# Optimization experiments

Measured on AMD Instinct MI355X. Metric: run time of the kernel, lower is better.

## Reference

```python
import math
import jax, jax.numpy as jnp
import numpy as np

B, T, C, H = 4, 2048, 1024, 16
HD = C // H  # 64


def setup_inputs() -> dict:
    key = jax.random.key(0)
    k1, k2, k3 = jax.random.split(key, 3)
    x = jax.random.normal(k1, (B, T, C), dtype=jnp.float32)
    w_attn = jax.random.normal(k2, (3 * C, C), dtype=jnp.float32) * 0.02
    w_proj = jax.random.normal(k3, (C, C), dtype=jnp.float32) * 0.02
    return {"x": x, "w_attn": w_attn, "w_proj": w_proj}


def _rms_norm(x):
    # F.rms_norm with no weight; eps defaults to dtype eps
    eps = jnp.finfo(x.dtype).eps
    return x * jax.lax.rsqrt(jnp.mean(x * x, axis=-1, keepdims=True) + eps)


def _rotary_cos_sin(seq_len, dim):
    inv_freq = 1.0 / (10000.0 ** (jnp.arange(0, dim, 2, dtype=jnp.float32) / dim))
    t = jnp.arange(seq_len, dtype=jnp.float32)
    freqs = jnp.outer(t, inv_freq)  # (T, dim//2)
    # original caches cos/sin in bfloat16
    return jnp.cos(freqs).astype(jnp.bfloat16), jnp.sin(freqs).astype(jnp.bfloat16)


def _apply_rotary(x, cos, sin):
    # x: (B, T, H, hd); cos/sin: (T, hd//2), broadcast over batch and heads
    half = x.shape[-1] // 2
    x1, x2 = x[..., :half], x[..., half:]
    c = cos[None, :, None, :].astype(x.dtype)
    s = sin[None, :, None, :].astype(x.dtype)
    y1 = x1 * c + x2 * s
    y2 = -x1 * s + x2 * c
    return jnp.concatenate([y1, y2], axis=-1)


def _forward(x, w_attn, w_proj):
    Bx, Tx, Cx = x.shape
    qkv = x @ w_attn.T  # (B, T, 3C)
    q, k, v = jnp.split(qkv, 3, axis=-1)
    q = q.reshape(Bx, Tx, H, HD)
    k = k.reshape(Bx, Tx, H, HD)
    v = v.reshape(Bx, Tx, H, HD)
    # qk RMSNorm then RoPE (nanogpt-style)
    q = _rms_norm(q)
    k = _rms_norm(k)
    cos, sin = _rotary_cos_sin(Tx, HD)
    q = _apply_rotary(q, cos, sin)
    k = _apply_rotary(k, cos, sin)
    # causal euclidean attention (custom_attention, mode='euc', dropout_p=0)
    scale = 1.0 / math.sqrt(HD)
    scores = jnp.einsum('bqhd,bkhd->bhqk', q, k) * scale  # (B, H, T, T)
    causal = jnp.tril(jnp.ones((Tx, Tx), dtype=bool))
    scores = jnp.where(causal[None, None, :, :], scores, -jnp.inf)
    attn = jax.nn.softmax(scores, axis=-1)
    y = jnp.einsum('bhqk,bkhd->bqhd', attn, v).reshape(Bx, Tx, Cx)
    return y @ w_proj.T


def reference(x, w_attn, w_proj):
    return _forward(x, w_attn, w_proj)
```

## Files before the change

kernel.cpp:

```cpp
#include <hip/hip_runtime.h>

typedef unsigned short u16;
typedef unsigned int u32;
typedef __attribute__((ext_vector_type(4))) int v4i;
typedef __attribute__((ext_vector_type(4))) float f32x4;
typedef __attribute__((ext_vector_type(16))) float f32x16;
typedef __attribute__((ext_vector_type(4))) u16 v4u;
typedef __attribute__((ext_vector_type(2))) u32 u32x2;
typedef __attribute__((ext_vector_type(8))) __bf16 bf16x8;

#define B_ 4
#define T_ 2048
#define C_ 1024
#define H_ 16
#define HD_ 64
#define C3_ 3072

__device__ __forceinline__ u16 f2b(float f) {
    unsigned u = __builtin_bit_cast(unsigned, f);
    u += 0x7FFFu + ((u >> 16) & 1u);
    return (u16)(u >> 16);
}
__device__ __forceinline__ float b2f(u16 h) {
    unsigned u = ((unsigned)h) << 16;
    return __builtin_bit_cast(float, u);
}
__device__ __forceinline__ u32 pk2(float lo, float hi) {
    __bf16 a = (__bf16)lo, b = (__bf16)hi;
    return (u32)__builtin_bit_cast(u16, a) | ((u32)__builtin_bit_cast(u16, b) << 16);
}
__device__ __forceinline__ void glds16(const u16* g, u16* l) {
    __builtin_amdgcn_global_load_lds((const __attribute__((address_space(1))) void*)g,
                                     (__attribute__((address_space(3))) void*)l, 16, 0, 0);
}

__global__ __launch_bounds__(256) void cast_f32_bf16(const float* __restrict__ in,
                                                     u16* __restrict__ out, int n4) {
    int i = blockIdx.x * 256 + threadIdx.x;
    if (i >= n4) return;
    f32x4 v = *(const f32x4*)(in + (size_t)i * 4);
    v4u o;
    o[0] = f2b(v[0]); o[1] = f2b(v[1]); o[2] = f2b(v[2]); o[3] = f2b(v[3]);
    *(v4u*)(out + (size_t)i * 4) = o;
}

__global__ __launch_bounds__(256) void rope_tab(u16* __restrict__ rope) {
    int id = blockIdx.x * 256 + threadIdx.x;
    int t = id >> 5, j = id & 31;
    float invf = exp2f(-(float)j * (13.287712379549449f / 32.0f));
    float fr = (float)t * invf;
    float s, c;
    sincosf(fr, &s, &c);
    rope[id * 2]     = f2b(c);
    rope[id * 2 + 1] = f2b(s);
}

__device__ __forceinline__ void store_out(u16* p, float v)   { *p = f2b(v); }
__device__ __forceinline__ void store_out(float* p, float v) { *p = v; }

template <typename OutT>
__global__ __launch_bounds__(256) void gemm_bt5(const u16* __restrict__ A, const u16* __restrict__ Bm,
                                                OutT* __restrict__ Cout, int Mdim, int Ndim, int Kdim) {
    __shared__ u16 As[8192];
    __shared__ u16 Bs[8192];
    const int tid = threadIdx.x;
    const int F = blockIdx.y * gridDim.x + blockIdx.x;
    const int cpx = (gridDim.x * gridDim.y) >> 3;
    const int wg = (F & 7) * cpx + (F >> 3);
    const int row0 = (wg / gridDim.x) * 128;
    const int col0 = (wg % gridDim.x) * 128;
    const int w = tid >> 6, lane = tid & 63;
    const int wm = w >> 1, wn = w & 1;
    const int lr = lane & 15, lk = lane >> 4;

    const f32x4 zf = {0.f, 0.f, 0.f, 0.f};
    f32x4 acc[4][4];
#pragma unroll
    for (int m = 0; m < 4; m++)
#pragma unroll
        for (int n = 0; n < 4; n++) acc[m][n] = zf;

    const u16* Ab = A + (size_t)row0 * Kdim;
    const u16* Bb = Bm + (size_t)col0 * Kdim;
    const int srw = lane >> 3;
    const int gch = (lane & 7) ^ (srw & 7);
    const size_t grow[4] = {
        (size_t)(w * 32 + 0 * 8 + srw) * Kdim + gch * 8,
        (size_t)(w * 32 + 1 * 8 + srw) * Kdim + gch * 8,
        (size_t)(w * 32 + 2 * 8 + srw) * Kdim + gch * 8,
        (size_t)(w * 32 + 3 * 8 + srw) * Kdim + gch * 8 };
    const int rx = lr & 7;

    for (int k0 = 0; k0 < Kdim; k0 += 64) {
#pragma unroll
        for (int j = 0; j < 4; j++) glds16(Ab + grow[j] + k0, As + (w * 32 + j * 8) * 64);
#pragma unroll
        for (int j = 0; j < 4; j++) glds16(Bb + grow[j] + k0, Bs + (w * 32 + j * 8) * 64);
        __syncthreads();
#pragma unroll
        for (int kk = 0; kk < 2; kk++) {
            const int chx = ((kk * 4 + lk) ^ rx) * 8;
            bf16x8 af[4], bfr[4];
#pragma unroll
            for (int m = 0; m < 4; m++) af[m]  = *(const bf16x8*)&As[(wm * 64 + m * 16 + lr) * 64 + chx];
#pragma unroll
            for (int n = 0; n < 4; n++) bfr[n] = *(const bf16x8*)&Bs[(wn * 64 + n * 16 + lr) * 64 + chx];
#pragma unroll
            for (int m = 0; m < 4; m++)
#pragma unroll
                for (int n = 0; n < 4; n++)
                    acc[m][n] = __builtin_amdgcn_mfma_f32_16x16x32_bf16(af[m], bfr[n], acc[m][n], 0, 0, 0);
        }
        __syncthreads();
    }
#pragma unroll
    for (int m = 0; m < 4; m++)
#pragma unroll
        for (int n = 0; n < 4; n++) {
            const int rr = row0 + wm * 64 + m * 16 + lk * 4;
            const int cc = col0 + wn * 64 + n * 16 + lr;
#pragma unroll
            for (int j = 0; j < 4; j++)
                store_out(Cout + (size_t)(rr + j) * Ndim + cc, acc[m][n][j]);
        }
}

__global__ __launch_bounds__(256) void gemm_bt6(const u16* __restrict__ A, const u16* __restrict__ Bm,
                                                float* __restrict__ Cout, int Mdim, int Ndim, int Kdim) {
    __shared__ u16 As[8192];
    __shared__ u16 Bs[4096];
    const int tid = threadIdx.x;
    const int F = blockIdx.y * gridDim.x + blockIdx.x;
    const int cpx = (gridDim.x * gridDim.y) >> 3;
    const int wg = (F & 7) * cpx + (F >> 3);
    const int row0 = (wg / gridDim.x) * 128;
    const int col0 = (wg % gridDim.x) * 64;
    const int w = tid >> 6, lane = tid & 63;
    const int wm = w >> 1, wn = w & 1;
    const int lr = lane & 15, lk = lane >> 4;

    const f32x4 zf = {0.f, 0.f, 0.f, 0.f};
    f32x4 acc[4][2];
#pragma unroll
    for (int m = 0; m < 4; m++)
#pragma unroll
        for (int n = 0; n < 2; n++) acc[m][n] = zf;

    const u16* Ab = A + (size_t)row0 * Kdim;
    const u16* Bb = Bm + (size_t)col0 * Kdim;
    const int srw = lane >> 3;
    const int gch = (lane & 7) ^ (srw & 7);
    const size_t growA[4] = {
        (size_t)(w * 32 + 0 * 8 + srw) * Kdim + gch * 8,
        (size_t)(w * 32 + 1 * 8 + srw) * Kdim + gch * 8,
        (size_t)(w * 32 + 2 * 8 + srw) * Kdim + gch * 8,
        (size_t)(w * 32 + 3 * 8 + srw) * Kdim + gch * 8 };
    const size_t growB[2] = {
        (size_t)(w * 16 + 0 * 8 + srw) * Kdim + gch * 8,
        (size_t)(w * 16 + 1 * 8 + srw) * Kdim + gch * 8 };
    const int rx = lr & 7;

    for (int k0 = 0; k0 < Kdim; k0 += 64) {
#pragma unroll
        for (int j = 0; j < 4; j++) glds16(Ab + growA[j] + k0, As + (w * 32 + j * 8) * 64);
#pragma unroll
        for (int j = 0; j < 2; j++) glds16(Bb + growB[j] + k0, Bs + (w * 16 + j * 8) * 64);
        __syncthreads();
#pragma unroll
        for (int kk = 0; kk < 2; kk++) {
            const int chx = ((kk * 4 + lk) ^ rx) * 8;
            bf16x8 af[4], bfr[2];
#pragma unroll
            for (int m = 0; m < 4; m++) af[m]  = *(const bf16x8*)&As[(wm * 64 + m * 16 + lr) * 64 + chx];
#pragma unroll
            for (int n = 0; n < 2; n++) bfr[n] = *(const bf16x8*)&Bs[(wn * 32 + n * 16 + lr) * 64 + chx];
#pragma unroll
            for (int m = 0; m < 4; m++)
#pragma unroll
                for (int n = 0; n < 2; n++)
                    acc[m][n] = __builtin_amdgcn_mfma_f32_16x16x32_bf16(af[m], bfr[n], acc[m][n], 0, 0, 0);
        }
        __syncthreads();
    }
#pragma unroll
    for (int m = 0; m < 4; m++)
#pragma unroll
        for (int n = 0; n < 2; n++) {
            const int rr = row0 + wm * 64 + m * 16 + lk * 4;
            const int cc = col0 + wn * 32 + n * 16 + lr;
#pragma unroll
            for (int j = 0; j < 4; j++)
                Cout[(size_t)(rr + j) * Ndim + cc] = acc[m][n][j];
        }
}

__global__ __launch_bounds__(256) void norm_rope3(const u16* __restrict__ qkv, u16* __restrict__ Qn,
                                                  u16* __restrict__ Kn, u16* __restrict__ Vt,
                                                  const u16* __restrict__ rope) {
    __shared__ u16 sl[32][72];
    const int tid = threadIdx.x, bid = blockIdx.x;
    const int tt = bid & 63, bh = bid >> 6;
    const int b = bh >> 4, h = bh & 15;
    const int rl = tid >> 3, g = tid & 7;
    const int t = tt * 32 + rl;
    const size_t rowbase = ((size_t)(b * T_) + t) * C3_ + h * HD_;
    const size_t obase = ((size_t)bh * T_ + t) * HD_ + g * 8;
    *(v4i*)&sl[rl][g * 8] = *(const v4i*)(qkv + rowbase + 2 * C_ + g * 8);
    const u16* rp = rope + (size_t)t * 64;
#pragma unroll
    for (int p = 0; p < 2; p++) {
        v4i rw = *(const v4i*)(qkv + rowbase + p * C_ + g * 8);
        float xv[8];
#pragma unroll
        for (int c = 0; c < 4; c++) {
            unsigned u = (unsigned)rw[c];
            xv[c * 2]     = b2f((u16)(u & 0xFFFFu));
            xv[c * 2 + 1] = b2f((u16)(u >> 16));
        }
        float ss = 0.f;
#pragma unroll
        for (int j = 0; j < 8; j++) ss += xv[j] * xv[j];
        ss += __shfl_xor(ss, 1, 64);
        ss += __shfl_xor(ss, 2, 64);
        ss += __shfl_xor(ss, 4, 64);
        const float rms = rsqrtf(ss * (1.f / 64.f) + 1.1920929e-7f);
        const float oscale = p == 0 ? 0.18033688011112042f : 1.0f;
#pragma unroll
        for (int j = 0; j < 8; j++) xv[j] *= rms;
        float xp[8];
#pragma unroll
        for (int j = 0; j < 8; j++) xp[j] = __shfl_xor(xv[j], 4, 64);
        float ys[8];
        if (g < 4) {
#pragma unroll
            for (int j = 0; j < 8; j++) {
                int d = g * 8 + j;
                ys[j] = xv[j] * b2f(rp[d * 2]) + xp[j] * b2f(rp[d * 2 + 1]);
            }
        } else {
#pragma unroll
            for (int j = 0; j < 8; j++) {
                int dd = (g - 4) * 8 + j;
                ys[j] = xv[j] * b2f(rp[dd * 2]) - xp[j] * b2f(rp[dd * 2 + 1]);
            }
        }
        v4i ov;
#pragma unroll
        for (int c = 0; c < 4; c++)
            ov[c] = (int)((unsigned)f2b(ys[c * 2] * oscale) | ((unsigned)f2b(ys[c * 2 + 1] * oscale) << 16));
        *(v4i*)((p ? Kn : Qn) + obase) = ov;
    }
    __syncthreads();
    const int d = tid >> 2, tq = tid & 3;
    v4i ov;
#pragma unroll
    for (int c = 0; c < 4; c++)
        ov[c] = (int)((unsigned)sl[tq * 8 + c * 2][d] | ((unsigned)sl[tq * 8 + c * 2 + 1][d] << 16));
    *(v4i*)(Vt + ((size_t)bh * HD_ + d) * T_ + tt * 32 + tq * 8) = ov;
}

__global__ __launch_bounds__(256, 4) void attn_fwd11(const u16* __restrict__ Qn, const u16* __restrict__ Kn,
                                                     const u16* __restrict__ Vt, u16* __restrict__ Yb) {
    __shared__ u16 Ks[2][4096];
    __shared__ u16 Vs[2][4096];
    const int tid = threadIdx.x;
    const int w = tid >> 6, lane = tid & 63, la = lane & 31, hi = lane >> 5;
    const int gid = blockIdx.x;
    const int bh = gid & 63, qb = 15 - (gid >> 6);
    const int b = bh >> 4, h = bh & 15;
    const int q0w = qb * 128 + w * 32;
    const int q = q0w + la;
    const u16* Qp = Qn + (size_t)bh * T_ * HD_;
    const u16* Kp = Kn + (size_t)bh * T_ * HD_;
    const u16* Vp = Vt + (size_t)bh * HD_ * T_;

    bf16x8 qf[4];
#pragma unroll
    for (int c = 0; c < 4; c++)
        qf[c] = *(const bf16x8*)(Qp + (size_t)q * HD_ + c * 16 + hi * 8);

    v4i oi; oi[0] = oi[1] = oi[2] = oi[3] = 0x3F803F80;
    const bf16x8 onesf = __builtin_bit_cast(bf16x8, oi);

    f32x16 O0, O1, lsum;
#pragma unroll
    for (int r = 0; r < 16; r++) { O0[r] = 0.f; O1[r] = 0.f; lsum[r] = 0.f; }
    const int lastt = q0w >> 6;
    const int ntile = 2 * qb + 2;
    const int s8 = lane >> 3;
    const int gch = (lane & 7) ^ s8;
    const int Rw = w * 16;
    const size_t kbase = (size_t)(Rw + s8) * HD_ + gch * 8;
    const size_t vbase = (size_t)(Rw + s8) * T_ + gch * 8;
    const int swl = (la & 7) << 3;

    auto STAGE = [&](int bi, int kv0) {
        glds16(Kp + kbase + (size_t)kv0 * HD_,       &Ks[bi][Rw * 64]);
        glds16(Kp + kbase + (size_t)(kv0 + 8) * HD_, &Ks[bi][Rw * 64 + 512]);
        glds16(Vp + vbase + kv0,                     &Vs[bi][Rw * 64]);
        glds16(Vp + vbase + 8 * T_ + kv0,            &Vs[bi][Rw * 64 + 512]);
    };
    auto COMPUTE = [&](int bi, int kt) {
        __builtin_amdgcn_s_setprio(1);
        const int kv0 = kt * 64;
        f32x16 s0, s1;
#pragma unroll
        for (int r = 0; r < 16; r++) { s0[r] = 0.f; s1[r] = 0.f; }
#pragma unroll
        for (int c = 0; c < 4; c++) {
            const int cb = c * 16 + hi * 8;
            bf16x8 kfa = *(const bf16x8*)&Ks[bi][la * 64 + (cb ^ swl)];
            bf16x8 kfb = *(const bf16x8*)&Ks[bi][(32 + la) * 64 + (cb ^ swl)];
            s0 = __builtin_amdgcn_mfma_f32_32x32x16_bf16(kfa, qf[c], s0, 0, 0, 0);
            s1 = __builtin_amdgcn_mfma_f32_32x32x16_bf16(kfb, qf[c], s1, 0, 0, 0);
        }
        if (kt == lastt) {
#pragma unroll
            for (int r = 0; r < 16; r++) {
                const int cr = (r & 3) + 8 * (r >> 2) + 4 * hi;
                if (kv0 + cr > q)      s0[r] = -3e38f;
                if (kv0 + 32 + cr > q) s1[r] = -3e38f;
            }
        }
        float p0[16], p1[16];
#pragma unroll
        for (int r = 0; r < 16; r++) {
            p0[r] = exp2f(s0[r]);
            p1[r] = exp2f(s1[r]);
        }
#pragma unroll
        for (int g = 0; g < 2; g++) {
            u32 P2[8];
#pragma unroll
            for (int j = 0; j < 8; j++)
                P2[j] = g ? pk2(p1[2 * j], p1[2 * j + 1]) : pk2(p0[2 * j], p0[2 * j + 1]);
            auto s02 = __builtin_amdgcn_permlane32_swap((int)P2[0], (int)P2[2], false, false);
            auto s13 = __builtin_amdgcn_permlane32_swap((int)P2[1], (int)P2[3], false, false);
            auto s46 = __builtin_amdgcn_permlane32_swap((int)P2[4], (int)P2[6], false, false);
            auto s57 = __builtin_amdgcn_permlane32_swap((int)P2[5], (int)P2[7], false, false);
            v4i w0, w1;
            w0[0] = s02[0]; w0[1] = s13[0]; w0[2] = s02[1]; w0[3] = s13[1];
            w1[0] = s46[0]; w1[1] = s57[0]; w1[2] = s46[1]; w1[3] = s57[1];
            const bf16x8 pa0 = __builtin_bit_cast(bf16x8, w0);
            const bf16x8 pa1 = __builtin_bit_cast(bf16x8, w1);
            lsum = __builtin_amdgcn_mfma_f32_32x32x16_bf16(onesf, pa0, lsum, 0, 0, 0);
            lsum = __builtin_amdgcn_mfma_f32_32x32x16_bf16(onesf, pa1, lsum, 0, 0, 0);
#pragma unroll
            for (int ks = 0; ks < 2; ks++) {
                const bf16x8 pa = ks ? pa1 : pa0;
                const int cb = g * 32 + ks * 16 + hi * 8;
                bf16x8 vfa = *(const bf16x8*)&Vs[bi][la * 64 + (cb ^ swl)];
                bf16x8 vfb = *(const bf16x8*)&Vs[bi][(32 + la) * 64 + (cb ^ swl)];
                O0 = __builtin_amdgcn_mfma_f32_32x32x16_bf16(vfa, pa, O0, 0, 0, 0);
                O1 = __builtin_amdgcn_mfma_f32_32x32x16_bf16(vfb, pa, O1, 0, 0, 0);
            }
        }
        __builtin_amdgcn_s_setprio(0);
    };

    STAGE(0, 0);
    for (int t = 0; t < ntile; t += 2) {
        __syncthreads();
        STAGE(1, (t + 1) * 64);
        if (t <= lastt) COMPUTE(0, t);
        __syncthreads();
        if (t + 2 < ntile) STAGE(0, (t + 2) * 64);
        if (t + 1 <= lastt) COMPUTE(1, t + 1);
    }

    const float inv = 1.f / lsum[0];
    u16* yrow = Yb + ((size_t)(b * T_) + q) * C_ + h * HD_;
#pragma unroll
    for (int r4 = 0; r4 < 4; r4++) {
        u32x2 st0, st1;
        st0[0] = pk2(O0[r4 * 4 + 0] * inv, O0[r4 * 4 + 1] * inv);
        st0[1] = pk2(O0[r4 * 4 + 2] * inv, O0[r4 * 4 + 3] * inv);
        st1[0] = pk2(O1[r4 * 4 + 0] * inv, O1[r4 * 4 + 1] * inv);
        st1[1] = pk2(O1[r4 * 4 + 2] * inv, O1[r4 * 4 + 3] * inv);
        *(u32x2*)(yrow + r4 * 8 + hi * 4)      = st0;
        *(u32x2*)(yrow + 32 + r4 * 8 + hi * 4) = st1;
    }
}

extern "C" void kernel_launch(void* const* d_in, const int* in_sizes, int n_in,
                              void* d_out, int out_size, void* d_ws, size_t ws_size,
                              hipStream_t stream) {
    const float* x      = (const float*)d_in[0];
    const float* w_attn = (const float*)d_in[1];
    const float* w_proj = (const float*)d_in[2];
    float* out = (float*)d_out;
    char* ws = (char*)d_ws;
    u16* Wpb = (u16*)(ws + 0);
    u16* Rp  = (u16*)(ws + 2097152);
    u16* Xb  = (u16*)(ws + 2359296);
    u16* Wab = (u16*)(ws + 19136512);
    u16* QKV = (u16*)(ws + 25427968);
    u16* Qn  = (u16*)(ws + 2359296);
    u16* Kn  = (u16*)(ws + 75759616);
    u16* Vt  = (u16*)(ws + 92536832);
    u16* Yb  = (u16*)(ws + 25427968);

    cast_f32_bf16<<<8192, 256, 0, stream>>>(x, Xb, 2097152);
    cast_f32_bf16<<<3072, 256, 0, stream>>>(w_attn, Wab, 786432);
    cast_f32_bf16<<<1024, 256, 0, stream>>>(w_proj, Wpb, 262144);
    rope_tab<<<256, 256, 0, stream>>>(Rp);
    gemm_bt5<u16><<<dim3(24, 64), 256, 0, stream>>>(Xb, Wab, QKV, 8192, 3072, 1024);
    norm_rope3<<<4096, 256, 0, stream>>>(QKV, Qn, Kn, Vt, Rp);
    attn_fwd11<<<1024, 256, 0, stream>>>(Qn, Kn, Vt, Yb);
    gemm_bt6<<<dim3(16, 64), 256, 0, stream>>>(Yb, Wpb, out, 8192, 1024, 1024);
}
```

Before: 190.1 us.

## Fuse casts and rope table, fold norm/rope/V-transpose into QKV GEMM epilogue

Merges the three cast kernels and the rope table kernel into a single prep launch. The RMSNorm, RoPE, Q scaling and V transpose move into the QKV GEMM epilogue, so the bf16 QKV intermediate is never written and re-read. The attention kernel drops its setprio calls. The output projection switches to the 128x128 gemm_bt5 tile, which halves its grid. The epilogue now issues scattered 2-byte stores, the V-transpose stores are strided, and the larger projection tiles leave fewer blocks to fill the GPU.

```diff
diff --git a/kernel.cpp b/kernel.cpp
--- a/kernel.cpp
+++ b/kernel.cpp
@@ -34,25 +34,30 @@
                                      (__attribute__((address_space(3))) void*)l, 16, 0, 0);
 }
 
-__global__ __launch_bounds__(256) void cast_f32_bf16(const float* __restrict__ in,
-                                                     u16* __restrict__ out, int n4) {
-    int i = blockIdx.x * 256 + threadIdx.x;
-    if (i >= n4) return;
+__device__ __forceinline__ void cast4(const float* in, u16* out, int i) {
     f32x4 v = *(const f32x4*)(in + (size_t)i * 4);
     v4u o;
     o[0] = f2b(v[0]); o[1] = f2b(v[1]); o[2] = f2b(v[2]); o[3] = f2b(v[3]);
     *(v4u*)(out + (size_t)i * 4) = o;
 }
-
-__global__ __launch_bounds__(256) void rope_tab(u16* __restrict__ rope) {
-    int id = blockIdx.x * 256 + threadIdx.x;
-    int t = id >> 5, j = id & 31;
+__global__ __launch_bounds__(256) void prep(const float* __restrict__ x, const float* __restrict__ wa,
+                                            const float* __restrict__ wp, u16* __restrict__ Xb,
+                                            u16* __restrict__ Wab, u16* __restrict__ Wpb,
+                                            u16* __restrict__ Rp) {
+    int i = blockIdx.x * 256 + threadIdx.x;
+    if (i < 2097152) { cast4(x, Xb, i); return; }
+    i -= 2097152;
+    if (i < 786432) { cast4(wa, Wab, i); return; }
+    i -= 786432;
+    if (i < 262144) { cast4(wp, Wpb, i); return; }
+    i -= 262144;
+    int t = i >> 5, j = i & 31;
     float invf = exp2f(-(float)j * (13.287712379549449f / 32.0f));
     float fr = (float)t * invf;
     float s, c;
     sincosf(fr, &s, &c);
-    rope[id * 2]     = f2b(c);
-    rope[id * 2 + 1] = f2b(s);
+    Rp[i * 2]     = f2b(c);
+    Rp[i * 2 + 1] = f2b(s);
 }
 
 __device__ __forceinline__ void store_out(u16* p, float v)   { *p = f2b(v); }
@@ -125,142 +130,119 @@
         }
 }
 
-__global__ __launch_bounds__(256) void gemm_bt6(const u16* __restrict__ A, const u16* __restrict__ Bm,
-                                                float* __restrict__ Cout, int Mdim, int Ndim, int Kdim) {
+__global__ __launch_bounds__(256) void gemm_qkv(const u16* __restrict__ A, const u16* __restrict__ Bm,
+                                                u16* __restrict__ Qn, u16* __restrict__ Kn,
+                                                u16* __restrict__ Vt, const u16* __restrict__ rope) {
+    const int Kdim = 1024;
     __shared__ u16 As[8192];
-    __shared__ u16 Bs[4096];
+    __shared__ u16 Bs[8192];
     const int tid = threadIdx.x;
     const int F = blockIdx.y * gridDim.x + blockIdx.x;
     const int cpx = (gridDim.x * gridDim.y) >> 3;
     const int wg = (F & 7) * cpx + (F >> 3);
     const int row0 = (wg / gridDim.x) * 128;
-    const int col0 = (wg % gridDim.x) * 64;
+    const int col0 = (wg % gridDim.x) * 128;
     const int w = tid >> 6, lane = tid & 63;
     const int wm = w >> 1, wn = w & 1;
     const int lr = lane & 15, lk = lane >> 4;
 
     const f32x4 zf = {0.f, 0.f, 0.f, 0.f};
-    f32x4 acc[4][2];
+    f32x4 acc[4][4];
 #pragma unroll
     for (int m = 0; m < 4; m++)
 #pragma unroll
-        for (int n = 0; n < 2; n++) acc[m][n] = zf;
+        for (int n = 0; n < 4; n++) acc[m][n] = zf;
 
     const u16* Ab = A + (size_t)row0 * Kdim;
     const u16* Bb = Bm + (size_t)col0 * Kdim;
     const int srw = lane >> 3;
     const int gch = (lane & 7) ^ (srw & 7);
-    const size_t growA[4] = {
+    const size_t grow[4] = {
         (size_t)(w * 32 + 0 * 8 + srw) * Kdim + gch * 8,
         (size_t)(w * 32 + 1 * 8 + srw) * Kdim + gch * 8,
         (size_t)(w * 32 + 2 * 8 + srw) * Kdim + gch * 8,
         (size_t)(w * 32 + 3 * 8 + srw) * Kdim + gch * 8 };
-    const size_t growB[2] = {
-        (size_t)(w * 16 + 0 * 8 + srw) * Kdim + gch * 8,
-        (size_t)(w * 16 + 1 * 8 + srw) * Kdim + gch * 8 };
     const int rx = lr & 7;
 
     for (int k0 = 0; k0 < Kdim; k0 += 64) {
 #pragma unroll
-        for (int j = 0; j < 4; j++) glds16(Ab + growA[j] + k0, As + (w * 32 + j * 8) * 64);
-#pragma unroll
-        for (int j = 0; j < 2; j++) glds16(Bb + growB[j] + k0, Bs + (w * 16 + j * 8) * 64);
+        for (int j = 0; j < 4; j++) glds16(Ab + grow[j] + k0, As + (w * 32 + j * 8) * 64);
+#pragma unroll
+        for (int j = 0; j < 4; j++) glds16(Bb + grow[j] + k0, Bs + (w * 32 + j * 8) * 64);
         __syncthreads();
 #pragma unroll
         for (int kk = 0; kk < 2; kk++) {
             const int chx = ((kk * 4 + lk) ^ rx) * 8;
-            bf16x8 af[4], bfr[2];
+            bf16x8 af[4], bfr[4];
 #pragma unroll
             for (int m = 0; m < 4; m++) af[m]  = *(const bf16x8*)&As[(wm * 64 + m * 16 + lr) * 64 + chx];
 #pragma unroll
-            for (int n = 0; n < 2; n++) bfr[n] = *(const bf16x8*)&Bs[(wn * 32 + n * 16 + lr) * 64 + chx];
+            for (int n = 0; n < 4; n++) bfr[n] = *(const bf16x8*)&Bs[(wn * 64 + n * 16 + lr) * 64 + chx];
 #pragma unroll
             for (int m = 0; m < 4; m++)
 #pragma unroll
-                for (int n = 0; n < 2; n++)
+                for (int n = 0; n < 4; n++)
                     acc[m][n] = __builtin_amdgcn_mfma_f32_16x16x32_bf16(af[m], bfr[n], acc[m][n], 0, 0, 0);
         }
         __syncthreads();
     }
-#pragma unroll
-    for (int m = 0; m < 4; m++)
-#pragma unroll
-        for (int n = 0; n < 2; n++) {
-            const int rr = row0 + wm * 64 + m * 16 + lk * 4;
-            const int cc = col0 + wn * 32 + n * 16 + lr;
+    const u32* rp32 = (const u32*)rope;
+    const int type = col0 >> 10;
+    const int h = ((col0 & 1023) >> 6) + wn;
+    if (type == 2) {
+#pragma unroll
+        for (int m = 0; m < 4; m++)
+#pragma unroll
+            for (int n = 0; n < 4; n++) {
+                const int d = n * 16 + lr;
+                const int rr0 = row0 + wm * 64 + m * 16 + lk * 4;
+                const int bq = rr0 >> 11, t0 = rr0 & 2047;
+                const int bh = bq * 16 + h;
+                u32x2 st;
+                st[0] = pk2(acc[m][n][0], acc[m][n][1]);
+                st[1] = pk2(acc[m][n][2], acc[m][n][3]);
+                *(u32x2*)(Vt + ((size_t)bh * HD_ + d) * T_ + t0) = st;
+            }
+    } else {
+        u16* outb = type ? Kn : Qn;
+        const float osc = type ? 1.0f : 0.18033688011112042f;
+#pragma unroll
+        for (int m = 0; m < 4; m++) {
+            float ssj[4], rmsj[4];
 #pragma unroll
             for (int j = 0; j < 4; j++)
-                Cout[(size_t)(rr + j) * Ndim + cc] = acc[m][n][j];
-        }
-}
-
-__global__ __launch_bounds__(256) void norm_rope3(const u16* __restrict__ qkv, u16* __restrict__ Qn,
-                                                  u16* __restrict__ Kn, u16* __restrict__ Vt,
-                                                  const u16* __restrict__ rope) {
-    __shared__ u16 sl[32][72];
-    const int tid = threadIdx.x, bid = blockIdx.x;
-    const int tt = bid & 63, bh = bid >> 6;
-    const int b = bh >> 4, h = bh & 15;
-    const int rl = tid >> 3, g = tid & 7;
-    const int t = tt * 32 + rl;
-    const size_t rowbase = ((size_t)(b * T_) + t) * C3_ + h * HD_;
-    const size_t obase = ((size_t)bh * T_ + t) * HD_ + g * 8;
-    *(v4i*)&sl[rl][g * 8] = *(const v4i*)(qkv + rowbase + 2 * C_ + g * 8);
-    const u16* rp = rope + (size_t)t * 64;
-#pragma unroll
-    for (int p = 0; p < 2; p++) {
-        v4i rw = *(const v4i*)(qkv + rowbase + p * C_ + g * 8);
-        float xv[8];
-#pragma unroll
-        for (int c = 0; c < 4; c++) {
-            unsigned u = (unsigned)rw[c];
-            xv[c * 2]     = b2f((u16)(u & 0xFFFFu));
-            xv[c * 2 + 1] = b2f((u16)(u >> 16));
-        }
-        float ss = 0.f;
-#pragma unroll
-        for (int j = 0; j < 8; j++) ss += xv[j] * xv[j];
-        ss += __shfl_xor(ss, 1, 64);
-        ss += __shfl_xor(ss, 2, 64);
-        ss += __shfl_xor(ss, 4, 64);
-        const float rms = rsqrtf(ss * (1.f / 64.f) + 1.1920929e-7f);
-        const float oscale = p == 0 ? 0.18033688011112042f : 1.0f;
-#pragma unroll
-        for (int j = 0; j < 8; j++) xv[j] *= rms;
-        float xp[8];
-#pragma unroll
-        for (int j = 0; j < 8; j++) xp[j] = __shfl_xor(xv[j], 4, 64);
-        float ys[8];
-        if (g < 4) {
-#pragma unroll
-            for (int j = 0; j < 8; j++) {
-                int d = g * 8 + j;
-                ys[j] = xv[j] * b2f(rp[d * 2]) + xp[j] * b2f(rp[d * 2 + 1]);
-            }
-        } else {
-#pragma unroll
-            for (int j = 0; j < 8; j++) {
-                int dd = (g - 4) * 8 + j;
-                ys[j] = xv[j] * b2f(rp[dd * 2]) - xp[j] * b2f(rp[dd * 2 + 1]);
-            }
-        }
-        v4i ov;
-#pragma unroll
-        for (int c = 0; c < 4; c++)
-            ov[c] = (int)((unsigned)f2b(ys[c * 2] * oscale) | ((unsigned)f2b(ys[c * 2 + 1] * oscale) << 16));
-        *(v4i*)((p ? Kn : Qn) + obase) = ov;
-    }
-    __syncthreads();
-    const int d = tid >> 2, tq = tid & 3;
-    v4i ov;
-#pragma unroll
-    for (int c = 0; c < 4; c++)
-        ov[c] = (int)((unsigned)sl[tq * 8 + c * 2][d] | ((unsigned)sl[tq * 8 + c * 2 + 1][d] << 16));
-    *(v4i*)(Vt + ((size_t)bh * HD_ + d) * T_ + tt * 32 + tq * 8) = ov;
-}
-
-__global__ __launch_bounds__(256, 4) void attn_fwd11(const u16* __restrict__ Qn, const u16* __restrict__ Kn,
-                                                     const u16* __restrict__ Vt, u16* __restrict__ Yb) {
+                ssj[j] = acc[m][0][j] * acc[m][0][j] + acc[m][1][j] * acc[m][1][j]
+                       + acc[m][2][j] * acc[m][2][j] + acc[m][3][j] * acc[m][3][j];
+#pragma unroll
+            for (int off = 1; off < 16; off <<= 1)
+#pragma unroll
+                for (int j = 0; j < 4; j++) ssj[j] += __shfl_xor(ssj[j], off, 64);
+#pragma unroll
+            for (int j = 0; j < 4; j++)
+                rmsj[j] = rsqrtf(ssj[j] * (1.f / 64.f) + 1.1920929e-7f) * osc;
+#pragma unroll
+            for (int n = 0; n < 2; n++)
+#pragma unroll
+                for (int j = 0; j < 4; j++) {
+                    const int d = n * 16 + lr;
+                    const int rr = row0 + wm * 64 + m * 16 + lk * 4 + j;
+                    const int bq = rr >> 11, t = rr & 2047;
+                    const int bh = bq * 16 + h;
+                    const u32 cs = rp32[t * 32 + d];
+                    const float c = b2f((u16)(cs & 0xFFFFu));
+                    const float s = b2f((u16)(cs >> 16));
+                    const float x1 = acc[m][n][j] * rmsj[j];
+                    const float x2 = acc[m][n + 2][j] * rmsj[j];
+                    u16* bp = outb + ((size_t)bh * T_ + t) * HD_;
+                    bp[d]      = f2b(x1 * c + x2 * s);
+                    bp[d + 32] = f2b(x2 * c - x1 * s);
+                }
+        }
+    }
+}
+
+__global__ __launch_bounds__(256, 4) void attn_fwd9(const u16* __restrict__ Qn, const u16* __restrict__ Kn,
+                                                    const u16* __restrict__ Vt, u16* __restrict__ Yb) {
     __shared__ u16 Ks[2][4096];
     __shared__ u16 Vs[2][4096];
     const int tid = threadIdx.x;
@@ -301,7 +283,6 @@
         glds16(Vp + vbase + 8 * T_ + kv0,            &Vs[bi][Rw * 64 + 512]);
     };
     auto COMPUTE = [&](int bi, int kt) {
-        __builtin_amdgcn_s_setprio(1);
         const int kv0 = kt * 64;
         f32x16 s0, s1;
 #pragma unroll
@@ -355,7 +336,6 @@
                 O1 = __builtin_amdgcn_mfma_f32_32x32x16_bf16(vfb, pa, O1, 0, 0, 0);
             }
         }
-        __builtin_amdgcn_s_setprio(0);
     };
 
     STAGE(0, 0);
@@ -394,18 +374,13 @@
     u16* Rp  = (u16*)(ws + 2097152);
     u16* Xb  = (u16*)(ws + 2359296);
     u16* Wab = (u16*)(ws + 19136512);
-    u16* QKV = (u16*)(ws + 25427968);
-    u16* Qn  = (u16*)(ws + 2359296);
-    u16* Kn  = (u16*)(ws + 75759616);
-    u16* Vt  = (u16*)(ws + 92536832);
-    u16* Yb  = (u16*)(ws + 25427968);
-
-    cast_f32_bf16<<<8192, 256, 0, stream>>>(x, Xb, 2097152);
-    cast_f32_bf16<<<3072, 256, 0, stream>>>(w_attn, Wab, 786432);
-    cast_f32_bf16<<<1024, 256, 0, stream>>>(w_proj, Wpb, 262144);
-    rope_tab<<<256, 256, 0, stream>>>(Rp);
-    gemm_bt5<u16><<<dim3(24, 64), 256, 0, stream>>>(Xb, Wab, QKV, 8192, 3072, 1024);
-    norm_rope3<<<4096, 256, 0, stream>>>(QKV, Qn, Kn, Vt, Rp);
-    attn_fwd11<<<1024, 256, 0, stream>>>(Qn, Kn, Vt, Yb);
-    gemm_bt6<<<dim3(16, 64), 256, 0, stream>>>(Yb, Wpb, out, 8192, 1024, 1024);
-}
+    u16* Qn  = (u16*)(ws + 25427968);
+    u16* Kn  = (u16*)(ws + 42205184);
+    u16* Vt  = (u16*)(ws + 58982400);
+    u16* Yb  = (u16*)(ws + 75759616);
+
+    prep<<<12544, 256, 0, stream>>>(x, w_attn, w_proj, Xb, Wab, Wpb, Rp);
+    gemm_qkv<<<dim3(24, 64), 256, 0, stream>>>(Xb, Wab, Qn, Kn, Vt, Rp);
+    attn_fwd9<<<1024, 256, 0, stream>>>(Qn, Kn, Vt, Yb);
+    gemm_bt5<float><<<dim3(8, 64), 256, 0, stream>>>(Yb, Wpb, out, 8192, 1024, 1024);
+}
```

New measurement: 175.1 us. 1.09x faster.
